# Kernel tuning notes

Measured on AMD Instinct MI355X. Metric: run time of the kernel, lower is better.

Reference implementation:

```python
import jax, jax.numpy as jnp
import numpy as np

EMB = 128
HEADS = 4
HEAD_DIM = 128  # concat=False: out_channels per head = embedding_dim
LAYERS = 4
BOARD_WIDTH = 8
FC1 = 64
NEG_SLOPE = 0.2  # GATv2 LeakyReLU default
N_CELLS = 200_000
N_PIECES = 100_000
N_EDGES = 500_000
N_GRAPHS = 256


def setup_inputs() -> dict:
    key = jax.random.key(0)
    ks = jax.random.split(key, 24)
    cell_x = jnp.zeros((N_CELLS,), jnp.int32)  # cell vocab size is 1
    piece_x = jax.random.randint(ks[0], (N_PIECES, 1), 0, 2, dtype=jnp.int32)
    edge_src = jax.random.randint(ks[1], (N_EDGES,), 0, N_PIECES, dtype=jnp.int32)
    edge_dst = jax.random.randint(ks[2], (N_EDGES,), 0, N_CELLS, dtype=jnp.int32)
    cell_batch = jnp.sort(jax.random.randint(ks[3], (N_CELLS,), 0, N_GRAPHS, dtype=jnp.int32))

    HD = HEADS * HEAD_DIM
    s_emb = 1.0
    s_lin = 1.0 / np.sqrt(EMB)
    cell_emb = jax.random.normal(ks[4], (1, EMB), jnp.float32) * s_emb
    piece_emb = jax.random.normal(ks[5], (2, EMB), jnp.float32) * s_emb
    W_l = jax.random.normal(ks[6], (LAYERS, EMB, HD), jnp.float32) * s_lin
    b_l = jnp.zeros((LAYERS, HD), jnp.float32)
    W_r = jax.random.normal(ks[7], (LAYERS, EMB, HD), jnp.float32) * s_lin
    b_r = jnp.zeros((LAYERS, HD), jnp.float32)
    att = jax.random.normal(ks[8], (LAYERS, HEADS, HEAD_DIM), jnp.float32) * (1.0 / np.sqrt(HEAD_DIM))
    conv_bias = jnp.zeros((LAYERS, EMB), jnp.float32)
    fc1_w = jax.random.normal(ks[9], (EMB, FC1), jnp.float32) * s_lin
    fc1_b = jnp.zeros((FC1,), jnp.float32)
    policy_w = jax.random.normal(ks[10], (FC1, BOARD_WIDTH), jnp.float32) * (1.0 / np.sqrt(FC1))
    policy_b = jnp.zeros((BOARD_WIDTH,), jnp.float32)
    value_w = jax.random.normal(ks[11], (FC1, 1), jnp.float32) * (1.0 / np.sqrt(FC1))
    value_b = jnp.zeros((1,), jnp.float32)
    return {
        "cell_x": cell_x, "piece_x": piece_x, "edge_src": edge_src,
        "edge_dst": edge_dst, "cell_batch": cell_batch,
        "cell_emb": cell_emb, "piece_emb": piece_emb,
        "W_l": W_l, "b_l": b_l, "W_r": W_r, "b_r": b_r,
        "att": att, "conv_bias": conv_bias,
        "fc1_w": fc1_w, "fc1_b": fc1_b,
        "policy_w": policy_w, "policy_b": policy_b,
        "value_w": value_w, "value_b": value_b,
    }


def _gatv2_layer(piece, cell, edge_src, edge_dst, Wl, bl, Wr, br, a, bias):
    P, C = piece.shape[0], cell.shape[0]
    x_src = (piece @ Wl + bl).reshape(P, HEADS, HEAD_DIM)
    x_dst = (cell @ Wr + br).reshape(C, HEADS, HEAD_DIM)
    xs = x_src[edge_src]                       # [E,H,D] gather
    e = jax.nn.leaky_relu(xs + x_dst[edge_dst], NEG_SLOPE)
    logits = jnp.einsum('ehd,hd->eh', e, a)    # [E,H]
    # segment softmax over edges sharing the same destination cell
    m = jax.ops.segment_max(logits, edge_dst, num_segments=C)
    ex = jnp.exp(logits - m[edge_dst])
    denom = jax.ops.segment_sum(ex, edge_dst, num_segments=C)
    alpha = ex / denom[edge_dst]               # [E,H]
    msg = xs * alpha[:, :, None]               # [E,H,D]
    out = jax.ops.segment_sum(msg, edge_dst, num_segments=C)  # [C,H,D]
    return out.mean(axis=1) + bias             # concat=False -> mean over heads


def reference(cell_x, piece_x, edge_src, edge_dst, cell_batch,
              cell_emb, piece_emb, W_l, b_l, W_r, b_r, att, conv_bias,
              fc1_w, fc1_b, policy_w, policy_b, value_w, value_b):
    cell = cell_emb[cell_x]                    # [C,128]
    piece = piece_emb[piece_x.squeeze(-1)]     # [P,128], never updated (HeteroConv only emits dst type)
    for l in range(LAYERS):
        cell = _gatv2_layer(piece, cell, edge_src, edge_dst,
                            W_l[l], b_l[l], W_r[l], b_r[l], att[l], conv_bias[l])
        cell = jax.nn.relu(cell)               # dropout: eval-mode identity
    # global mean pool over cells per graph
    sums = jax.ops.segment_sum(cell, cell_batch, num_segments=N_GRAPHS)
    cnts = jax.ops.segment_sum(jnp.ones((cell.shape[0],), cell.dtype), cell_batch, num_segments=N_GRAPHS)
    graph_emb = sums / jnp.maximum(cnts, 1.0)[:, None]
    h = jax.nn.relu(graph_emb @ fc1_w + fc1_b)
    policy_logits = h @ policy_w + policy_b
    value = jnp.tanh(h @ value_w + value_b)
    return (policy_logits, value)
```

## Files before the change

### kernel.cpp

```cpp
#include <hip/hip_runtime.h>
#include <math.h>

#define NC 200000
#define NE 500000
#define NG 256
#define NLAYERS 4
#define NKEY 256
#define CLAMP 15
#define NSLOPE 0.2f
#define SB 256
#define CAP 48

#define O_STAGE 0u
#define O_TAILS 12582912u
#define O_XS    12845056u
#define O_TAB   12861440u

__device__ __forceinline__ float lrelu(float x) { return x > 0.f ? x : NSLOPE * x; }

__global__ void __launch_bounds__(512)
k_scatxs(const int* __restrict__ piece_x,
         const int* __restrict__ esrc,
         const int* __restrict__ edst,
         const int* __restrict__ cell_batch,
         const float* __restrict__ piece_emb,
         const float* __restrict__ W_l,
         const float* __restrict__ b_l,
         int* __restrict__ stage, int* __restrict__ tails,
         float* __restrict__ xs) {
  int tid = threadIdx.x, bid = blockIdx.x;
  if (bid < SB) {
    __shared__ int lt[NG];
    if (tid < NG) lt[tid] = 0;
    __syncthreads();
    int gid = bid * 512 + tid;
    if (gid < NE / 4) {
      int4 s4 = ((const int4*)esrc)[gid];
      int4 d4 = ((const int4*)edst)[gid];
      #pragma unroll
      for (int k = 0; k < 4; ++k) {
        int s = k == 0 ? s4.x : k == 1 ? s4.y : k == 2 ? s4.z : s4.w;
        int d = k == 0 ? d4.x : k == 1 ? d4.y : k == 2 ? d4.z : d4.w;
        int t = piece_x[s] & 1;
        int g = cell_batch[d];
        int pos = atomicAdd(&lt[g], 1);
        if (pos < CAP) stage[(g * SB + bid) * CAP + pos] = (d << 1) | t;
      }
    }
    __syncthreads();
    if (tid < NG) tails[tid * SB + bid] = min(lt[tid], CAP);
  } else {
    int idx = (bid - SB) * 512 + tid;
    if (idx < 4096) {
      int l = idx >> 10, t = (idx >> 9) & 1, j = idx & 511;
      float acc = b_l[l * 512 + j];
      const float* pe = piece_emb + t * 128;
      const float* W = W_l + l * 65536;
      #pragma unroll 8
      for (int d = 0; d < 128; ++d) acc = fmaf(pe[d], W[d * 512 + j], acc);
      xs[idx] = acc;
    }
  }
}

__global__ void __launch_bounds__(512)
k_layers(const float* __restrict__ cell_emb,
         const float* __restrict__ W_r, const float* __restrict__ b_r,
         const float* __restrict__ xs,  const float* __restrict__ att,
         const float* __restrict__ conv_bias,
         float* __restrict__ tab) {
  __shared__ float scell[128];
  __shared__ float part[8][2];
  __shared__ float wgt[8];
  int tid = threadIdx.x;
  int key = blockIdx.x, n0 = key >> 4, n1 = key & 15;
  if (tid < 128) scell[tid] = cell_emb[tid];
  __syncthreads();
  for (int l = 0; l < NLAYERS; ++l) {
    const float* Wl  = W_r + (size_t)l * 65536;
    const float* xsL = xs + l * 1024;
    float acc = b_r[l * 512 + tid];
    #pragma unroll 16
    for (int d = 0; d < 128; ++d)
      acc = fmaf(scell[d], Wl[d * 512 + tid], acc);
    float av = att[l * 512 + tid];
    float p0 = lrelu(xsL[tid] + acc) * av;
    float p1 = lrelu(xsL[512 + tid] + acc) * av;
    #pragma unroll
    for (int m = 32; m >= 1; m >>= 1) {
      p0 += __shfl_xor(p0, m);
      p1 += __shfl_xor(p1, m);
    }
    int w = tid >> 6, lane = tid & 63;
    if (lane == 0) { part[w][0] = p0; part[w][1] = p1; }
    __syncthreads();
    if (tid < 4) {
      float L0 = part[2 * tid][0] + part[2 * tid + 1][0];
      float L1 = part[2 * tid][1] + part[2 * tid + 1][1];
      float ww0 = 0.f, ww1 = 0.f;
      if (n0 + n1 > 0) {
        float m = -1e30f;
        if (n0 > 0) m = L0;
        if (n1 > 0) m = fmaxf(m, L1);
        float e0 = (n0 > 0) ? (float)n0 * expf(L0 - m) : 0.f;
        float e1 = (n1 > 0) ? (float)n1 * expf(L1 - m) : 0.f;
        float inv = 1.f / (e0 + e1);
        ww0 = e0 * inv; ww1 = e1 * inv;
      }
      wgt[tid] = ww0; wgt[4 + tid] = ww1;
    }
    __syncthreads();
    if (tid < 128) {
      float o = conv_bias[l * 128 + tid];
      #pragma unroll
      for (int h = 0; h < 4; ++h)
        o += 0.25f * (wgt[h]     * xsL[h * 128 + tid] +
                      wgt[4 + h] * xsL[512 + h * 128 + tid]);
      o = fmaxf(o, 0.f);
      scell[tid] = o;
      if (l == NLAYERS - 1) tab[key * 128 + tid] = o;
    }
    __syncthreads();
  }
}

__global__ void __launch_bounds__(256)
k_poolhead(const int* __restrict__ cell_batch,
           const int* __restrict__ stage, const int* __restrict__ tails,
           const float* __restrict__ tab,
           const float* __restrict__ fc1_w, const float* __restrict__ fc1_b,
           const float* __restrict__ pol_w, const float* __restrict__ pol_b,
           const float* __restrict__ val_w, const float* __restrict__ val_b,
           float* __restrict__ out) {
  __shared__ unsigned cnt[512];
  __shared__ int hist[NKEY];
  __shared__ int klist[NKEY];
  __shared__ int wcnt[4];
  __shared__ float emb[128];
  __shared__ float hbuf[64];
  int g = blockIdx.x, tid = threadIdx.x;
  cnt[tid] = 0; cnt[tid + 256] = 0; hist[tid] = 0;
  int lo = 0, hi = NC;
  while (lo < hi) { int mid = (lo + hi) >> 1; if (cell_batch[mid] < g) lo = mid + 1; else hi = mid; }
  int lo2 = lo, hi2 = NC;
  while (lo2 < hi2) { int mid = (lo2 + hi2) >> 1; if (cell_batch[mid] < g + 1) lo2 = mid + 1; else hi2 = mid; }
  int ncell = lo2 - lo;
  __syncthreads();
  {
    int t = tails[g * SB + tid];
    const int* seg = stage + (g * SB + tid) * CAP;
    for (int i = 0; i < t; ++i) {
      int e = seg[i];
      int lc = (e >> 1) - lo;
      lc = min(max(lc, 0), 1023);
      atomicAdd(&cnt[lc >> 1], 1u << (((lc & 1) * 2 + (e & 1)) * 8));
    }
  }
  __syncthreads();
  for (int c = tid; c < ncell; c += 256) {
    unsigned v = (cnt[c >> 1] >> ((c & 1) * 16)) & 0xffffu;
    int n0 = min((int)(v & 0xffu), CLAMP);
    int n1 = min((int)(v >> 8), CLAMP);
    atomicAdd(&hist[(n0 << 4) | n1], 1);
  }
  __syncthreads();
  unsigned long long m = __ballot(hist[tid] != 0);
  int w = tid >> 6, lane = tid & 63;
  if (lane == 0) wcnt[w] = __popcll(m);
  __syncthreads();
  int basep = 0;
  #pragma unroll
  for (int i = 0; i < 4; ++i) if (i < w) basep += wcnt[i];
  if (hist[tid] != 0)
    klist[basep + __popcll(m & ((1ull << lane) - 1ull))] = tid;
  __syncthreads();
  int kn = wcnt[0] + wcnt[1] + wcnt[2] + wcnt[3];
  if (tid < 128) {
    float acc = 0.f;
    for (int i = 0; i < kn; ++i) {
      int k = klist[i];
      acc = fmaf((float)hist[k], tab[k * 128 + tid], acc);
    }
    emb[tid] = acc / fmaxf((float)ncell, 1.f);
  }
  __syncthreads();
  if (tid < 64) {
    float a = fc1_b[tid];
    #pragma unroll 8
    for (int d = 0; d < 128; ++d) a = fmaf(emb[d], fc1_w[d * 64 + tid], a);
    hbuf[tid] = fmaxf(a, 0.f);
  }
  __syncthreads();
  if (tid < 8) {
    float p = pol_b[tid];
    #pragma unroll
    for (int k = 0; k < 64; ++k) p = fmaf(hbuf[k], pol_w[k * 8 + tid], p);
    out[g * 8 + tid] = p;
  } else if (tid == 8) {
    float v = val_b[0];
    #pragma unroll
    for (int k = 0; k < 64; ++k) v = fmaf(hbuf[k], val_w[k], v);
    out[NG * 8 + g] = tanhf(v);
  }
}

extern "C" void kernel_launch(void* const* d_in, const int* in_sizes, int n_in,
                              void* d_out, int out_size, void* d_ws, size_t ws_size,
                              hipStream_t stream) {
  (void)in_sizes; (void)n_in; (void)out_size; (void)ws_size;
  const int*   piece_x   = (const int*)d_in[1];
  const int*   edge_src  = (const int*)d_in[2];
  const int*   edge_dst  = (const int*)d_in[3];
  const int*   cell_batch= (const int*)d_in[4];
  const float* cell_emb  = (const float*)d_in[5];
  const float* piece_emb = (const float*)d_in[6];
  const float* W_l       = (const float*)d_in[7];
  const float* b_l       = (const float*)d_in[8];
  const float* W_r       = (const float*)d_in[9];
  const float* b_r       = (const float*)d_in[10];
  const float* att       = (const float*)d_in[11];
  const float* conv_bias = (const float*)d_in[12];
  const float* fc1_w     = (const float*)d_in[13];
  const float* fc1_b     = (const float*)d_in[14];
  const float* pol_w     = (const float*)d_in[15];
  const float* pol_b     = (const float*)d_in[16];
  const float* val_w     = (const float*)d_in[17];
  const float* val_b     = (const float*)d_in[18];
  float* out = (float*)d_out;

  char* ws = (char*)d_ws;
  int*   stage = (int*)(ws + O_STAGE);
  int*   tails = (int*)(ws + O_TAILS);
  float* xs    = (float*)(ws + O_XS);
  float* tab   = (float*)(ws + O_TAB);

  k_scatxs<<<SB + 8, 512, 0, stream>>>(piece_x, edge_src, edge_dst, cell_batch,
                                       piece_emb, W_l, b_l, stage, tails, xs);
  k_layers<<<NKEY, 512, 0, stream>>>(cell_emb, W_r, b_r, xs, att, conv_bias, tab);
  k_poolhead<<<NG, 256, 0, stream>>>(cell_batch, stage, tails, tab,
                                     fc1_w, fc1_b, pol_w, pol_b,
                                     val_w, val_b, out);
}
```

Baseline: 54.34 us.

## Fuse per-key layer table computation into the edge scatter kernel

Merges the layer-table kernel into the edge-scatter kernel by adding 256 extra blocks that each compute their key's four-layer GATv2 recurrence. Each of those blocks recomputes the piece-side projections (xs) from W_l itself instead of reading them from a separate precomputed buffer. This removes one kernel launch and the dependency between the two kernels, so table computation overlaps with the edge scatter. The cost is redundant W_l work across 256 blocks and doubled weight traffic per block.

```diff
diff --git a/kernel.cpp b/kernel.cpp
--- a/kernel.cpp
+++ b/kernel.cpp
@@ -13,21 +13,22 @@
 
 #define O_STAGE 0u
 #define O_TAILS 12582912u
-#define O_XS    12845056u
-#define O_TAB   12861440u
+#define O_TAB   12845056u
 
 __device__ __forceinline__ float lrelu(float x) { return x > 0.f ? x : NSLOPE * x; }
 
 __global__ void __launch_bounds__(512)
-k_scatxs(const int* __restrict__ piece_x,
-         const int* __restrict__ esrc,
-         const int* __restrict__ edst,
-         const int* __restrict__ cell_batch,
-         const float* __restrict__ piece_emb,
-         const float* __restrict__ W_l,
-         const float* __restrict__ b_l,
-         int* __restrict__ stage, int* __restrict__ tails,
-         float* __restrict__ xs) {
+k_scatlayers(const int* __restrict__ piece_x,
+             const int* __restrict__ esrc,
+             const int* __restrict__ edst,
+             const int* __restrict__ cell_batch,
+             const float* __restrict__ cell_emb,
+             const float* __restrict__ piece_emb,
+             const float* __restrict__ W_l, const float* __restrict__ b_l,
+             const float* __restrict__ W_r, const float* __restrict__ b_r,
+             const float* __restrict__ att, const float* __restrict__ conv_bias,
+             int* __restrict__ stage, int* __restrict__ tails,
+             float* __restrict__ tab) {
   int tid = threadIdx.x, bid = blockIdx.x;
   if (bid < SB) {
     __shared__ int lt[NG];
@@ -50,77 +51,69 @@
     __syncthreads();
     if (tid < NG) tails[tid * SB + bid] = min(lt[tid], CAP);
   } else {
-    int idx = (bid - SB) * 512 + tid;
-    if (idx < 4096) {
-      int l = idx >> 10, t = (idx >> 9) & 1, j = idx & 511;
-      float acc = b_l[l * 512 + j];
-      const float* pe = piece_emb + t * 128;
-      const float* W = W_l + l * 65536;
+    __shared__ float scell[128];
+    __shared__ float pe[256];
+    __shared__ float sxs0[512], sxs1[512];
+    __shared__ float part[8][2];
+    __shared__ float wgt[8];
+    int key = bid - SB, n0 = key >> 4, n1 = key & 15;
+    if (tid < 128) scell[tid] = cell_emb[tid];
+    else if (tid < 384) pe[tid - 128] = piece_emb[tid - 128];
+    __syncthreads();
+    for (int l = 0; l < NLAYERS; ++l) {
+      const float* Wl = W_l + (size_t)l * 65536;
+      const float* Wr = W_r + (size_t)l * 65536;
+      float xs0 = b_l[l * 512 + tid];
+      float xs1 = xs0;
+      float acc = b_r[l * 512 + tid];
       #pragma unroll 8
-      for (int d = 0; d < 128; ++d) acc = fmaf(pe[d], W[d * 512 + j], acc);
-      xs[idx] = acc;
-    }
-  }
-}
-
-__global__ void __launch_bounds__(512)
-k_layers(const float* __restrict__ cell_emb,
-         const float* __restrict__ W_r, const float* __restrict__ b_r,
-         const float* __restrict__ xs,  const float* __restrict__ att,
-         const float* __restrict__ conv_bias,
-         float* __restrict__ tab) {
-  __shared__ float scell[128];
-  __shared__ float part[8][2];
-  __shared__ float wgt[8];
-  int tid = threadIdx.x;
-  int key = blockIdx.x, n0 = key >> 4, n1 = key & 15;
-  if (tid < 128) scell[tid] = cell_emb[tid];
-  __syncthreads();
-  for (int l = 0; l < NLAYERS; ++l) {
-    const float* Wl  = W_r + (size_t)l * 65536;
-    const float* xsL = xs + l * 1024;
-    float acc = b_r[l * 512 + tid];
-    #pragma unroll 16
-    for (int d = 0; d < 128; ++d)
-      acc = fmaf(scell[d], Wl[d * 512 + tid], acc);
-    float av = att[l * 512 + tid];
-    float p0 = lrelu(xsL[tid] + acc) * av;
-    float p1 = lrelu(xsL[512 + tid] + acc) * av;
-    #pragma unroll
-    for (int m = 32; m >= 1; m >>= 1) {
-      p0 += __shfl_xor(p0, m);
-      p1 += __shfl_xor(p1, m);
-    }
-    int w = tid >> 6, lane = tid & 63;
-    if (lane == 0) { part[w][0] = p0; part[w][1] = p1; }
-    __syncthreads();
-    if (tid < 4) {
-      float L0 = part[2 * tid][0] + part[2 * tid + 1][0];
-      float L1 = part[2 * tid][1] + part[2 * tid + 1][1];
-      float ww0 = 0.f, ww1 = 0.f;
-      if (n0 + n1 > 0) {
-        float m = -1e30f;
-        if (n0 > 0) m = L0;
-        if (n1 > 0) m = fmaxf(m, L1);
-        float e0 = (n0 > 0) ? (float)n0 * expf(L0 - m) : 0.f;
-        float e1 = (n1 > 0) ? (float)n1 * expf(L1 - m) : 0.f;
-        float inv = 1.f / (e0 + e1);
-        ww0 = e0 * inv; ww1 = e1 * inv;
-      }
-      wgt[tid] = ww0; wgt[4 + tid] = ww1;
-    }
-    __syncthreads();
-    if (tid < 128) {
-      float o = conv_bias[l * 128 + tid];
+      for (int d = 0; d < 128; ++d) {
+        float wl = Wl[d * 512 + tid];
+        float wr = Wr[d * 512 + tid];
+        xs0 = fmaf(pe[d], wl, xs0);
+        xs1 = fmaf(pe[128 + d], wl, xs1);
+        acc = fmaf(scell[d], wr, acc);
+      }
+      sxs0[tid] = xs0; sxs1[tid] = xs1;
+      float av = att[l * 512 + tid];
+      float p0 = lrelu(xs0 + acc) * av;
+      float p1 = lrelu(xs1 + acc) * av;
       #pragma unroll
-      for (int h = 0; h < 4; ++h)
-        o += 0.25f * (wgt[h]     * xsL[h * 128 + tid] +
-                      wgt[4 + h] * xsL[512 + h * 128 + tid]);
-      o = fmaxf(o, 0.f);
-      scell[tid] = o;
-      if (l == NLAYERS - 1) tab[key * 128 + tid] = o;
-    }
-    __syncthreads();
+      for (int m = 32; m >= 1; m >>= 1) {
+        p0 += __shfl_xor(p0, m);
+        p1 += __shfl_xor(p1, m);
+      }
+      int w = tid >> 6, lane = tid & 63;
+      if (lane == 0) { part[w][0] = p0; part[w][1] = p1; }
+      __syncthreads();
+      if (tid < 4) {
+        float L0 = part[2 * tid][0] + part[2 * tid + 1][0];
+        float L1 = part[2 * tid][1] + part[2 * tid + 1][1];
+        float ww0 = 0.f, ww1 = 0.f;
+        if (n0 + n1 > 0) {
+          float m = -1e30f;
+          if (n0 > 0) m = L0;
+          if (n1 > 0) m = fmaxf(m, L1);
+          float e0 = (n0 > 0) ? (float)n0 * expf(L0 - m) : 0.f;
+          float e1 = (n1 > 0) ? (float)n1 * expf(L1 - m) : 0.f;
+          float inv = 1.f / (e0 + e1);
+          ww0 = e0 * inv; ww1 = e1 * inv;
+        }
+        wgt[tid] = ww0; wgt[4 + tid] = ww1;
+      }
+      __syncthreads();
+      if (tid < 128) {
+        float o = conv_bias[l * 128 + tid];
+        #pragma unroll
+        for (int h = 0; h < 4; ++h)
+          o += 0.25f * (wgt[h]     * sxs0[h * 128 + tid] +
+                        wgt[4 + h] * sxs1[h * 128 + tid]);
+        o = fmaxf(o, 0.f);
+        scell[tid] = o;
+        if (l == NLAYERS - 1) tab[key * 128 + tid] = o;
+      }
+      __syncthreads();
+    }
   }
 }
 
@@ -231,12 +224,12 @@
   char* ws = (char*)d_ws;
   int*   stage = (int*)(ws + O_STAGE);
   int*   tails = (int*)(ws + O_TAILS);
-  float* xs    = (float*)(ws + O_XS);
   float* tab   = (float*)(ws + O_TAB);
 
-  k_scatxs<<<SB + 8, 512, 0, stream>>>(piece_x, edge_src, edge_dst, cell_batch,
-                                       piece_emb, W_l, b_l, stage, tails, xs);
-  k_layers<<<NKEY, 512, 0, stream>>>(cell_emb, W_r, b_r, xs, att, conv_bias, tab);
+  k_scatlayers<<<SB + NKEY, 512, 0, stream>>>(piece_x, edge_src, edge_dst,
+                                              cell_batch, cell_emb, piece_emb,
+                                              W_l, b_l, W_r, b_r, att, conv_bias,
+                                              stage, tails, tab);
   k_poolhead<<<NG, 256, 0, stream>>>(cell_batch, stage, tails, tab,
                                      fc1_w, fc1_b, pol_w, pol_b,
                                      val_w, val_b, out);
```

After: 56.03 us. +3.1%, slower.
